# Performance work log

Measured on AMD Instinct MI355X. Metric: run time of the kernel, lower is better.

## Reference

```python
import jax, jax.numpy as jnp
import numpy as np

# NF4 codebook (bitsandbytes nf4 quant_type), 16 levels in [-1, 1]
NF4 = jnp.array([
    -1.0, -0.6961928009986877, -0.5250730514526367, -0.39491748809814453,
    -0.28444138169288635, -0.18477343022823334, -0.09105003625154495, 0.0,
    0.07958029955625534, 0.16093020141124725, 0.24611230194568634,
    0.33791524171829224, 0.44070982933044434, 0.5626170039176941,
    0.7229568362236023, 1.0], dtype=jnp.float32)
BLOCK = 64  # bitsandbytes default quant block size

TOKENS, HD, M = 8192, 4096, 11008


def dequant_nf4(codes, scales):
    # codes: [out, in] int in [0,16); scales: [out, in//BLOCK] per-block absmax
    out_f, in_f = codes.shape
    w = NF4[codes].reshape(out_f, in_f // BLOCK, BLOCK) * scales[:, :, None]
    return w.reshape(out_f, in_f)


def setup_inputs() -> dict:
    key = jax.random.key(0)
    k = jax.random.split(key, 7)
    return {
        "x": jax.random.normal(k[0], (TOKENS, HD), dtype=jnp.float32),
        "gate_codes": jax.random.randint(k[1], (M, HD), 0, 16, dtype=jnp.int32),
        "gate_scales": jax.random.uniform(k[2], (M, HD // BLOCK), dtype=jnp.float32) * 0.1,
        "up_codes": jax.random.randint(k[3], (M, HD), 0, 16, dtype=jnp.int32),
        "up_scales": jax.random.uniform(k[4], (M, HD // BLOCK), dtype=jnp.float32) * 0.1,
        "down_codes": jax.random.randint(k[5], (HD, M), 0, 16, dtype=jnp.int32),
        "down_scales": jax.random.uniform(k[6], (HD, M // BLOCK), dtype=jnp.float32) * 0.1,
    }


def reference(x, gate_codes, gate_scales, up_codes, up_scales, down_codes, down_scales):
    Wg = dequant_nf4(gate_codes, gate_scales)   # [m, hd]
    Wu = dequant_nf4(up_codes, up_scales)       # [m, hd]
    Wd = dequant_nf4(down_codes, down_scales)   # [hd, m]
    g = jnp.einsum('td,md->tm', x, Wg)          # gate_proj(x)
    u = jnp.einsum('td,md->tm', x, Wu)          # up_proj(x)
    h = jax.nn.silu(g) * u                      # SwiGLU
    return jnp.einsum('tm,dm->td', h, Wd)       # down_proj
```

## Files before the change

kernel.cpp:

```cpp
#include <hip/hip_runtime.h>
#include <hip/hip_bf16.h>

typedef _Float16 half8 __attribute__((ext_vector_type(8)));
typedef float floatx4 __attribute__((ext_vector_type(4)));

__device__ __constant__ float NF4_TAB[16] = {
    -1.0f, -0.6961928009986877f, -0.5250730514526367f, -0.39491748809814453f,
    -0.28444138169288635f, -0.18477343022823334f, -0.09105003625154495f, 0.0f,
    0.07958029955625534f, 0.16093020141124725f, 0.24611230194568634f,
    0.33791524171829224f, 0.44070982933044434f, 0.5626170039176941f,
    0.7229568362236023f, 1.0f};

typedef __attribute__((address_space(3))) void lds_t;
typedef __attribute__((address_space(1))) void gbl_t;

__device__ __forceinline__ void gload16(const void* g, void* l) {
  __builtin_amdgcn_global_load_lds((gbl_t*)g, (lds_t*)l, 16, 0, 0);
}

__global__ void cvt_f32_to_f16(const float* __restrict__ in,
                               _Float16* __restrict__ out, int total8) {
  int stride = gridDim.x * blockDim.x;
  for (int i = blockIdx.x * blockDim.x + threadIdx.x; i < total8; i += stride) {
    long e = (long)i * 8;
    const float4* ip = reinterpret_cast<const float4*>(in + e);
    float4 a = ip[0], b = ip[1];
    half8 o;
    o[0] = (_Float16)a.x; o[1] = (_Float16)a.y;
    o[2] = (_Float16)a.z; o[3] = (_Float16)a.w;
    o[4] = (_Float16)b.x; o[5] = (_Float16)b.y;
    o[6] = (_Float16)b.z; o[7] = (_Float16)b.w;
    *reinterpret_cast<half8*>(out + e) = o;
  }
}

__global__ void dequant_nf4(const int* __restrict__ codes,
                            const float* __restrict__ scales,
                            _Float16* __restrict__ out,
                            int total8, int C, int CB) {
  __shared__ float lut[16];
  if (threadIdx.x < 16) lut[threadIdx.x] = NF4_TAB[threadIdx.x];
  __syncthreads();
  int stride = gridDim.x * blockDim.x;
  for (int i = blockIdx.x * blockDim.x + threadIdx.x; i < total8; i += stride) {
    long e = (long)i * 8;
    int row = (int)(e / C);
    int col = (int)(e - (long)row * C);
    float sc = scales[row * CB + (col >> 6)];
    const int4* cp = reinterpret_cast<const int4*>(codes + e);
    int4 c0 = cp[0];
    int4 c1 = cp[1];
    half8 o;
    o[0] = (_Float16)(lut[c0.x & 15] * sc);
    o[1] = (_Float16)(lut[c0.y & 15] * sc);
    o[2] = (_Float16)(lut[c0.z & 15] * sc);
    o[3] = (_Float16)(lut[c0.w & 15] * sc);
    o[4] = (_Float16)(lut[c1.x & 15] * sc);
    o[5] = (_Float16)(lut[c1.y & 15] * sc);
    o[6] = (_Float16)(lut[c1.z & 15] * sc);
    o[7] = (_Float16)(lut[c1.w & 15] * sc);
    *reinterpret_cast<half8*>(out + e) = o;
  }
}

template <int K, int N, int EPI>
__global__ __launch_bounds__(512, 2) void gemm256(
    const _Float16* __restrict__ A,
    const _Float16* __restrict__ B,
    _Float16* __restrict__ GH,
    float* __restrict__ OUT) {
  constexpr int NT = K / 32;
  constexpr int NBC = N / 256;
  constexpr int NWG = (8192 / 256) * NBC;
  __shared__ __align__(16) _Float16 lds[3 * 16384];

  const int t = threadIdx.x;
  const int lane = t & 63;
  const int wave = t >> 6;
  const int wm = wave >> 2;
  const int wn = wave & 3;

  int bid = blockIdx.x;
  bid = (bid & 7) * (NWG >> 3) + (bid >> 3);
  const int bm = bid / NBC, bn = bid % NBC;

  const int lc = (t & 3) ^ ((t >> 3) & 3);
  const _Float16* pA0 = A + ((long)bm * 256 + (t >> 2)) * K + lc * 8;
  const _Float16* pA1 = pA0 + (long)128 * K;
  const _Float16* pB0 = B + ((long)bn * 256 + (t >> 2)) * K + lc * 8;
  const _Float16* pB1 = pB0 + (long)128 * K;
  const int dA0 = t * 8, dA1 = 4096 + t * 8;
  const int dB0 = 8192 + t * 8, dB1 = 12288 + t * 8;

  const int rA = wm * 128 + (lane & 15);
  const int rB = wn * 64 + (lane & 15);
  const int ckA = ((lane >> 4) ^ ((rA >> 1) & 3)) * 8;
  const int ckB = ((lane >> 4) ^ ((rB >> 1) & 3)) * 8;
  const int offA = rA * 32 + ckA;
  const int offB = 8192 + rB * 32 + ckB;

  gload16(pA0, lds + dA0);
  gload16(pA1, lds + dA1);
  gload16(pB0, lds + dB0);
  gload16(pB1, lds + dB1);
  gload16(pA0 + 32, lds + 16384 + dA0);
  gload16(pA1 + 32, lds + 16384 + dA1);
  gload16(pB0 + 32, lds + 16384 + dB0);
  gload16(pB1 + 32, lds + 16384 + dB1);
  pA0 += 64; pA1 += 64; pB0 += 64; pB1 += 64;
  asm volatile("s_waitcnt vmcnt(4)" ::: "memory");
  asm volatile("s_barrier" ::: "memory");
  __builtin_amdgcn_sched_barrier(0);

  floatx4 acc[8][4] = {};
  int buf = 0;

  for (int kt = 0; kt < NT; ++kt) {
    const _Float16* lb = lds + buf * 16384;
    const int sbuf = (buf == 0) ? 2 : buf - 1;
    _Float16* sb = lds + sbuf * 16384;
    const bool doStage = (kt + 2 < NT);

    half8 b[4], a[8];
#pragma unroll
    for (int j = 0; j < 4; ++j)
      b[j] = *reinterpret_cast<const half8*>(&lb[offB + j * 512]);
#pragma unroll
    for (int i = 0; i < 8; ++i)
      a[i] = *reinterpret_cast<const half8*>(&lb[offA + i * 512]);
    if (doStage) {
      gload16(pA0, sb + dA0);
      gload16(pA1, sb + dA1);
    }
    asm volatile("s_barrier" ::: "memory");
    __builtin_amdgcn_sched_barrier(0);
    __builtin_amdgcn_s_setprio(1);
#pragma unroll
    for (int i = 0; i < 4; ++i)
#pragma unroll
      for (int j = 0; j < 4; ++j)
        acc[i][j] = __builtin_amdgcn_mfma_f32_16x16x32_f16(a[i], b[j], acc[i][j], 0, 0, 0);
    __builtin_amdgcn_s_setprio(0);
    asm volatile("s_barrier" ::: "memory");
    __builtin_amdgcn_sched_barrier(0);

    if (doStage) {
      gload16(pB0, sb + dB0);
      gload16(pB1, sb + dB1);
      pA0 += 32; pA1 += 32; pB0 += 32; pB1 += 32;
    }
    __builtin_amdgcn_s_setprio(1);
#pragma unroll
    for (int i = 4; i < 8; ++i)
#pragma unroll
      for (int j = 0; j < 4; ++j)
        acc[i][j] = __builtin_amdgcn_mfma_f32_16x16x32_f16(a[i], b[j], acc[i][j], 0, 0, 0);
    __builtin_amdgcn_s_setprio(0);
    if (doStage) {
      asm volatile("s_waitcnt vmcnt(4)" ::: "memory");
    } else if (kt + 1 < NT) {
      asm volatile("s_waitcnt vmcnt(0)" ::: "memory");
    }
    asm volatile("s_barrier" ::: "memory");
    __builtin_amdgcn_sched_barrier(0);
    buf = (buf == 2) ? 0 : buf + 1;
  }

  const int r0 = bm * 256 + wm * 128 + (lane >> 4) * 4;
  const int c0 = bn * 256 + wn * 64 + (lane & 15);
#pragma unroll
  for (int i = 0; i < 8; ++i) {
#pragma unroll
    for (int j = 0; j < 4; ++j) {
#pragma unroll
      for (int ii = 0; ii < 4; ++ii) {
        const long idx = (long)(r0 + i * 16 + ii) * N + (c0 + j * 16);
        if (EPI == 0) {
          GH[idx] = (_Float16)acc[i][j][ii];
        } else if (EPI == 1) {
          float u = acc[i][j][ii];
          float g = (float)GH[idx];
          GH[idx] = (_Float16)(g / (1.0f + __expf(-g)) * u);
        } else {
          OUT[idx] = acc[i][j][ii];
        }
      }
    }
  }
}

extern "C" void kernel_launch(void* const* d_in, const int* in_sizes, int n_in,
                              void* d_out, int out_size, void* d_ws, size_t ws_size,
                              hipStream_t stream) {
  const float* x           = (const float*)d_in[0];
  const int*   gate_codes  = (const int*)d_in[1];
  const float* gate_scales = (const float*)d_in[2];
  const int*   up_codes    = (const int*)d_in[3];
  const float* up_scales   = (const float*)d_in[4];
  const int*   down_codes  = (const int*)d_in[5];
  const float* down_scales = (const float*)d_in[6];
  float* out = (float*)d_out;

  const long T = 8192, HD = 4096, M = 11008;

  char* ws = (char*)d_ws;
  _Float16* x16 = (_Float16*)ws;
  _Float16* W   = (_Float16*)(ws + T * HD * 2);
  _Float16* gh  = (_Float16*)(ws + T * HD * 2 + M * HD * 2);

  cvt_f32_to_f16<<<2048, 256, 0, stream>>>(x, x16, (int)(T * HD / 8));

  dequant_nf4<<<2048, 256, 0, stream>>>(gate_codes, gate_scales, W,
                                        (int)(M * HD / 8), (int)HD, (int)(HD / 64));
  gemm256<4096, 11008, 0><<<(8192 / 256) * (11008 / 256), 512, 0, stream>>>(
      x16, W, gh, nullptr);

  dequant_nf4<<<2048, 256, 0, stream>>>(up_codes, up_scales, W,
                                        (int)(M * HD / 8), (int)HD, (int)(HD / 64));
  gemm256<4096, 11008, 1><<<(8192 / 256) * (11008 / 256), 512, 0, stream>>>(
      x16, W, gh, nullptr);

  dequant_nf4<<<2048, 256, 0, stream>>>(down_codes, down_scales, W,
                                        (int)(HD * M / 8), (int)M, (int)(M / 64));
  gemm256<11008, 4096, 2><<<(8192 / 256) * (4096 / 256), 512, 0, stream>>>(
      gh, W, nullptr, out);
}
```

Baseline: 2.341 ms.

## Restructure GEMM main loop into double-buffered 64-wide K tiles with four phases

Replaces the triple-buffered 32-wide K pipeline with a double buffer holding 64-wide K tiles, split into four compute phases per iteration. Each phase loads half of the B fragments and issues the A or B global-to-LDS stage for the next tile, interleaved with barriers. The aim is fewer loop iterations per K and finer-grained overlap of global loads with MFMA work. In exchange it adds more barriers and A-fragment reloads per iteration, and raises the LDS footprint, which may affect the 2-blocks-per-CU occupancy target.

```diff
diff --git a/kernel.cpp b/kernel.cpp
--- a/kernel.cpp
+++ b/kernel.cpp
@@ -69,10 +69,10 @@
     const _Float16* __restrict__ B,
     _Float16* __restrict__ GH,
     float* __restrict__ OUT) {
-  constexpr int NT = K / 32;
+  constexpr int NT = K / 64;
   constexpr int NBC = N / 256;
   constexpr int NWG = (8192 / 256) * NBC;
-  __shared__ __align__(16) _Float16 lds[3 * 16384];
+  __shared__ __align__(16) _Float16 lds[2 * 32768];
 
   const int t = threadIdx.x;
   const int lane = t & 63;
@@ -85,86 +85,116 @@
   const int bm = bid / NBC, bn = bid % NBC;
 
   const int lc = (t & 3) ^ ((t >> 3) & 3);
-  const _Float16* pA0 = A + ((long)bm * 256 + (t >> 2)) * K + lc * 8;
-  const _Float16* pA1 = pA0 + (long)128 * K;
-  const _Float16* pB0 = B + ((long)bn * 256 + (t >> 2)) * K + lc * 8;
-  const _Float16* pB1 = pB0 + (long)128 * K;
-  const int dA0 = t * 8, dA1 = 4096 + t * 8;
-  const int dB0 = 8192 + t * 8, dB1 = 12288 + t * 8;
+  const _Float16* gA = A + ((long)bm * 256 + (t >> 2)) * K + lc * 8;
+  const _Float16* gB = B + ((long)bn * 256 + (t >> 2)) * K + lc * 8;
+  const long rstep = (long)128 * K;
+  const int dst = t * 8;
 
   const int rA = wm * 128 + (lane & 15);
   const int rB = wn * 64 + (lane & 15);
   const int ckA = ((lane >> 4) ^ ((rA >> 1) & 3)) * 8;
   const int ckB = ((lane >> 4) ^ ((rB >> 1) & 3)) * 8;
   const int offA = rA * 32 + ckA;
-  const int offB = 8192 + rB * 32 + ckB;
-
-  gload16(pA0, lds + dA0);
-  gload16(pA1, lds + dA1);
-  gload16(pB0, lds + dB0);
-  gload16(pB1, lds + dB1);
-  gload16(pA0 + 32, lds + 16384 + dA0);
-  gload16(pA1 + 32, lds + 16384 + dA1);
-  gload16(pB0 + 32, lds + 16384 + dB0);
-  gload16(pB1 + 32, lds + 16384 + dB1);
-  pA0 += 64; pA1 += 64; pB0 += 64; pB1 += 64;
+  const int offB = 16384 + rB * 32 + ckB;
+
+#define STAGE_SLOT(gp, slab, koff, dbuf)                                   \
+  gload16((gp) + (koff), lds + (dbuf) * 32768 + (slab) + dst);             \
+  gload16((gp) + (koff) + rstep, lds + (dbuf) * 32768 + (slab) + dst + 4096);
+
+  STAGE_SLOT(gA, 0, 0, 0);
+  STAGE_SLOT(gB, 16384, 0, 0);
+  STAGE_SLOT(gA, 8192, 32, 0);
+  STAGE_SLOT(gB, 24576, 32, 0);
+  gA += 64; gB += 64;
   asm volatile("s_waitcnt vmcnt(4)" ::: "memory");
-  asm volatile("s_barrier" ::: "memory");
+  __builtin_amdgcn_s_barrier();
   __builtin_amdgcn_sched_barrier(0);
 
   floatx4 acc[8][4] = {};
-  int buf = 0;
 
   for (int kt = 0; kt < NT; ++kt) {
-    const _Float16* lb = lds + buf * 16384;
-    const int sbuf = (buf == 0) ? 2 : buf - 1;
-    _Float16* sb = lds + sbuf * 16384;
-    const bool doStage = (kt + 2 < NT);
-
-    half8 b[4], a[8];
-#pragma unroll
-    for (int j = 0; j < 4; ++j)
-      b[j] = *reinterpret_cast<const half8*>(&lb[offB + j * 512]);
+    const int cb = kt & 1;
+    const int sbuf = cb ^ 1;
+    const _Float16* lb = lds + cb * 32768;
+    const bool st = (kt + 1 < NT);
+    const bool last = (kt == NT - 1);
+
+    half8 a[8], b[2];
+
 #pragma unroll
     for (int i = 0; i < 8; ++i)
       a[i] = *reinterpret_cast<const half8*>(&lb[offA + i * 512]);
-    if (doStage) {
-      gload16(pA0, sb + dA0);
-      gload16(pA1, sb + dA1);
-    }
-    asm volatile("s_barrier" ::: "memory");
-    __builtin_amdgcn_sched_barrier(0);
-    __builtin_amdgcn_s_setprio(1);
-#pragma unroll
-    for (int i = 0; i < 4; ++i)
-#pragma unroll
-      for (int j = 0; j < 4; ++j)
-        acc[i][j] = __builtin_amdgcn_mfma_f32_16x16x32_f16(a[i], b[j], acc[i][j], 0, 0, 0);
-    __builtin_amdgcn_s_setprio(0);
-    asm volatile("s_barrier" ::: "memory");
-    __builtin_amdgcn_sched_barrier(0);
-
-    if (doStage) {
-      gload16(pB0, sb + dB0);
-      gload16(pB1, sb + dB1);
-      pA0 += 32; pA1 += 32; pB0 += 32; pB1 += 32;
-    }
-    __builtin_amdgcn_s_setprio(1);
-#pragma unroll
-    for (int i = 4; i < 8; ++i)
-#pragma unroll
-      for (int j = 0; j < 4; ++j)
-        acc[i][j] = __builtin_amdgcn_mfma_f32_16x16x32_f16(a[i], b[j], acc[i][j], 0, 0, 0);
-    __builtin_amdgcn_s_setprio(0);
-    if (doStage) {
-      asm volatile("s_waitcnt vmcnt(4)" ::: "memory");
-    } else if (kt + 1 < NT) {
-      asm volatile("s_waitcnt vmcnt(0)" ::: "memory");
-    }
-    asm volatile("s_barrier" ::: "memory");
-    __builtin_amdgcn_sched_barrier(0);
-    buf = (buf == 2) ? 0 : buf + 1;
-  }
+    b[0] = *reinterpret_cast<const half8*>(&lb[offB]);
+    b[1] = *reinterpret_cast<const half8*>(&lb[offB + 512]);
+    if (st) { STAGE_SLOT(gA, 0, 0, sbuf); }
+    __builtin_amdgcn_s_barrier();
+    asm volatile("s_waitcnt lgkmcnt(0)" ::: "memory");
+    __builtin_amdgcn_sched_barrier(0);
+    __builtin_amdgcn_s_setprio(1);
+#pragma unroll
+    for (int i = 0; i < 8; ++i) {
+      acc[i][0] = __builtin_amdgcn_mfma_f32_16x16x32_f16(a[i], b[0], acc[i][0], 0, 0, 0);
+      acc[i][1] = __builtin_amdgcn_mfma_f32_16x16x32_f16(a[i], b[1], acc[i][1], 0, 0, 0);
+    }
+    __builtin_amdgcn_s_setprio(0);
+    __builtin_amdgcn_s_barrier();
+    __builtin_amdgcn_sched_barrier(0);
+
+    b[0] = *reinterpret_cast<const half8*>(&lb[offB + 2 * 512]);
+    b[1] = *reinterpret_cast<const half8*>(&lb[offB + 3 * 512]);
+    if (st) { STAGE_SLOT(gB, 16384, 0, sbuf); }
+    if (last) { asm volatile("s_waitcnt vmcnt(0)" ::: "memory"); }
+    else      { asm volatile("s_waitcnt vmcnt(4)" ::: "memory"); }
+    __builtin_amdgcn_s_barrier();
+    asm volatile("s_waitcnt lgkmcnt(0)" ::: "memory");
+    __builtin_amdgcn_sched_barrier(0);
+    __builtin_amdgcn_s_setprio(1);
+#pragma unroll
+    for (int i = 0; i < 8; ++i) {
+      acc[i][2] = __builtin_amdgcn_mfma_f32_16x16x32_f16(a[i], b[0], acc[i][2], 0, 0, 0);
+      acc[i][3] = __builtin_amdgcn_mfma_f32_16x16x32_f16(a[i], b[1], acc[i][3], 0, 0, 0);
+    }
+    __builtin_amdgcn_s_setprio(0);
+    __builtin_amdgcn_s_barrier();
+    __builtin_amdgcn_sched_barrier(0);
+
+#pragma unroll
+    for (int i = 0; i < 8; ++i)
+      a[i] = *reinterpret_cast<const half8*>(&lb[8192 + offA + i * 512]);
+    b[0] = *reinterpret_cast<const half8*>(&lb[8192 + offB]);
+    b[1] = *reinterpret_cast<const half8*>(&lb[8192 + offB + 512]);
+    if (st) { STAGE_SLOT(gA, 8192, 32, sbuf); }
+    __builtin_amdgcn_s_barrier();
+    asm volatile("s_waitcnt lgkmcnt(0)" ::: "memory");
+    __builtin_amdgcn_sched_barrier(0);
+    __builtin_amdgcn_s_setprio(1);
+#pragma unroll
+    for (int i = 0; i < 8; ++i) {
+      acc[i][0] = __builtin_amdgcn_mfma_f32_16x16x32_f16(a[i], b[0], acc[i][0], 0, 0, 0);
+      acc[i][1] = __builtin_amdgcn_mfma_f32_16x16x32_f16(a[i], b[1], acc[i][1], 0, 0, 0);
+    }
+    __builtin_amdgcn_s_setprio(0);
+    __builtin_amdgcn_s_barrier();
+    __builtin_amdgcn_sched_barrier(0);
+
+    b[0] = *reinterpret_cast<const half8*>(&lb[8192 + offB + 2 * 512]);
+    b[1] = *reinterpret_cast<const half8*>(&lb[8192 + offB + 3 * 512]);
+    if (st) { STAGE_SLOT(gB, 24576, 32, sbuf); gA += 64; gB += 64; }
+    if (!last) { asm volatile("s_waitcnt vmcnt(4)" ::: "memory"); }
+    __builtin_amdgcn_s_barrier();
+    asm volatile("s_waitcnt lgkmcnt(0)" ::: "memory");
+    __builtin_amdgcn_sched_barrier(0);
+    __builtin_amdgcn_s_setprio(1);
+#pragma unroll
+    for (int i = 0; i < 8; ++i) {
+      acc[i][2] = __builtin_amdgcn_mfma_f32_16x16x32_f16(a[i], b[0], acc[i][2], 0, 0, 0);
+      acc[i][3] = __builtin_amdgcn_mfma_f32_16x16x32_f16(a[i], b[1], acc[i][3], 0, 0, 0);
+    }
+    __builtin_amdgcn_s_setprio(0);
+    __builtin_amdgcn_s_barrier();
+    __builtin_amdgcn_sched_barrier(0);
+  }
+#undef STAGE_SLOT
 
   const int r0 = bm * 256 + wm * 128 + (lane >> 4) * 4;
   const int c0 = bn * 256 + wn * 64 + (lane & 15);
```

After: 2.303 ms. Within noise of the previous version (-1.6%).

## Deepen GEMM LDS pipeline to four stages and split A-fragment loads

Applied to the files above, without the earlier changes.

Changes the GEMM's LDS ring from three to four stages, so tiles are prefetched three K-steps ahead, with vmcnt waits adjusted for the drain at the end. The A fragments are now read in two halves of four, each before its own MFMA half, which lowers the number of live A registers. The goal is to hide more global-load latency behind MFMA work. The cost is more LDS per block: 128KB is too much for two 512-thread blocks to share a CU, so occupancy likely drops to one block per CU. The sched_barrier calls are also replaced by plain compiler fences, which loosens scheduling control.

```diff
diff --git a/kernel.cpp b/kernel.cpp
--- a/kernel.cpp
+++ b/kernel.cpp
@@ -17,6 +17,8 @@
 __device__ __forceinline__ void gload16(const void* g, void* l) {
   __builtin_amdgcn_global_load_lds((gbl_t*)g, (lds_t*)l, 16, 0, 0);
 }
+
+#define FENCE() asm volatile("" ::: "memory")
 
 __global__ void cvt_f32_to_f16(const float* __restrict__ in,
                                _Float16* __restrict__ out, int total8) {
@@ -72,7 +74,7 @@
   constexpr int NT = K / 32;
   constexpr int NBC = N / 256;
   constexpr int NWG = (8192 / 256) * NBC;
-  __shared__ __align__(16) _Float16 lds[3 * 16384];
+  __shared__ __align__(16) _Float16 lds[4 * 16384];
 
   const int t = threadIdx.x;
   const int lane = t & 63;
@@ -85,12 +87,10 @@
   const int bm = bid / NBC, bn = bid % NBC;
 
   const int lc = (t & 3) ^ ((t >> 3) & 3);
-  const _Float16* pA0 = A + ((long)bm * 256 + (t >> 2)) * K + lc * 8;
-  const _Float16* pA1 = pA0 + (long)128 * K;
-  const _Float16* pB0 = B + ((long)bn * 256 + (t >> 2)) * K + lc * 8;
-  const _Float16* pB1 = pB0 + (long)128 * K;
-  const int dA0 = t * 8, dA1 = 4096 + t * 8;
-  const int dB0 = 8192 + t * 8, dB1 = 12288 + t * 8;
+  const _Float16* gA = A + ((long)bm * 256 + (t >> 2)) * K + lc * 8;
+  const _Float16* gB = B + ((long)bn * 256 + (t >> 2)) * K + lc * 8;
+  const long rstep = (long)128 * K;
+  const int dst = t * 8;
 
   const int rA = wm * 128 + (lane & 15);
   const int rB = wn * 64 + (lane & 15);
@@ -99,41 +99,38 @@
   const int offA = rA * 32 + ckA;
   const int offB = 8192 + rB * 32 + ckB;
 
-  gload16(pA0, lds + dA0);
-  gload16(pA1, lds + dA1);
-  gload16(pB0, lds + dB0);
-  gload16(pB1, lds + dB1);
-  gload16(pA0 + 32, lds + 16384 + dA0);
-  gload16(pA1 + 32, lds + 16384 + dA1);
-  gload16(pB0 + 32, lds + 16384 + dB0);
-  gload16(pB1 + 32, lds + 16384 + dB1);
-  pA0 += 64; pA1 += 64; pB0 += 64; pB1 += 64;
-  asm volatile("s_waitcnt vmcnt(4)" ::: "memory");
-  asm volatile("s_barrier" ::: "memory");
-  __builtin_amdgcn_sched_barrier(0);
+#define STAGE_A(dbuf) \
+  gload16(gA, lds + (dbuf) * 16384 + dst); \
+  gload16(gA + rstep, lds + (dbuf) * 16384 + dst + 4096); gA += 32;
+#define STAGE_B(dbuf) \
+  gload16(gB, lds + (dbuf) * 16384 + 8192 + dst); \
+  gload16(gB + rstep, lds + (dbuf) * 16384 + 8192 + dst + 4096); gB += 32;
+
+  STAGE_A(0); STAGE_B(0);
+  STAGE_A(1); STAGE_B(1);
+  STAGE_A(2); STAGE_B(2);
+  asm volatile("s_waitcnt vmcnt(8)" ::: "memory");
+  __builtin_amdgcn_s_barrier();
+  FENCE();
 
   floatx4 acc[8][4] = {};
-  int buf = 0;
 
   for (int kt = 0; kt < NT; ++kt) {
-    const _Float16* lb = lds + buf * 16384;
-    const int sbuf = (buf == 0) ? 2 : buf - 1;
-    _Float16* sb = lds + sbuf * 16384;
-    const bool doStage = (kt + 2 < NT);
-
-    half8 b[4], a[8];
+    const _Float16* lb = lds + (kt & 3) * 16384;
+    const int s3 = (kt + 3) & 3;
+    const bool st = (kt + 3 < NT);
+
+    half8 a[4], b[4];
+
+#pragma unroll
+    for (int i = 0; i < 4; ++i)
+      a[i] = *reinterpret_cast<const half8*>(&lb[offA + i * 512]);
 #pragma unroll
     for (int j = 0; j < 4; ++j)
       b[j] = *reinterpret_cast<const half8*>(&lb[offB + j * 512]);
-#pragma unroll
-    for (int i = 0; i < 8; ++i)
-      a[i] = *reinterpret_cast<const half8*>(&lb[offA + i * 512]);
-    if (doStage) {
-      gload16(pA0, sb + dA0);
-      gload16(pA1, sb + dA1);
-    }
-    asm volatile("s_barrier" ::: "memory");
-    __builtin_amdgcn_sched_barrier(0);
+    if (st) { STAGE_A(s3); }
+    __builtin_amdgcn_s_barrier();
+    FENCE();
     __builtin_amdgcn_s_setprio(1);
 #pragma unroll
     for (int i = 0; i < 4; ++i)
@@ -141,30 +138,30 @@
       for (int j = 0; j < 4; ++j)
         acc[i][j] = __builtin_amdgcn_mfma_f32_16x16x32_f16(a[i], b[j], acc[i][j], 0, 0, 0);
     __builtin_amdgcn_s_setprio(0);
-    asm volatile("s_barrier" ::: "memory");
-    __builtin_amdgcn_sched_barrier(0);
-
-    if (doStage) {
-      gload16(pB0, sb + dB0);
-      gload16(pB1, sb + dB1);
-      pA0 += 32; pA1 += 32; pB0 += 32; pB1 += 32;
-    }
+    __builtin_amdgcn_s_barrier();
+    FENCE();
+
+#pragma unroll
+    for (int i = 0; i < 4; ++i)
+      a[i] = *reinterpret_cast<const half8*>(&lb[offA + (4 + i) * 512]);
+    if (st) { STAGE_B(s3); }
+    if (kt < NT - 3)       { asm volatile("s_waitcnt vmcnt(8)" ::: "memory"); }
+    else if (kt == NT - 3) { asm volatile("s_waitcnt vmcnt(4)" ::: "memory"); }
+    else if (kt == NT - 2) { asm volatile("s_waitcnt vmcnt(0)" ::: "memory"); }
+    __builtin_amdgcn_s_barrier();
+    FENCE();
     __builtin_amdgcn_s_setprio(1);
 #pragma unroll
-    for (int i = 4; i < 8; ++i)
+    for (int i = 0; i < 4; ++i)
 #pragma unroll
       for (int j = 0; j < 4; ++j)
-        acc[i][j] = __builtin_amdgcn_mfma_f32_16x16x32_f16(a[i], b[j], acc[i][j], 0, 0, 0);
+        acc[4 + i][j] = __builtin_amdgcn_mfma_f32_16x16x32_f16(a[i], b[j], acc[4 + i][j], 0, 0, 0);
     __builtin_amdgcn_s_setprio(0);
-    if (doStage) {
-      asm volatile("s_waitcnt vmcnt(4)" ::: "memory");
-    } else if (kt + 1 < NT) {
-      asm volatile("s_waitcnt vmcnt(0)" ::: "memory");
-    }
-    asm volatile("s_barrier" ::: "memory");
-    __builtin_amdgcn_sched_barrier(0);
-    buf = (buf == 2) ? 0 : buf + 1;
-  }
+    __builtin_amdgcn_s_barrier();
+    FENCE();
+  }
+#undef STAGE_A
+#undef STAGE_B
 
   const int r0 = bm * 256 + wm * 128 + (lane >> 4) * 4;
   const int c0 = bn * 256 + wn * 64 + (lane & 15);
```

Measured after the change: 2.381 ms. About the same (+1.7%).
